# Performance work log

Hardware: AMD Instinct MI355X
Metric: run time of the kernel (lower is better)

Reference implementation:

```python
import jax, jax.numpy as jnp
from jax import lax
import numpy as np

GROUPS = 32

def setup_inputs() -> dict:
    key = jax.random.key(0)
    ks = jax.random.split(key, 12)
    B, C, H, O, N = 4, 256, 256, 256, 4096
    s = 0.02  # small init scale to keep logits in a stable range
    x  = jax.random.normal(ks[0], (B, C, N), dtype=jnp.float32)
    Wk = jax.random.normal(ks[1], (H, C), dtype=jnp.float32) * s
    bk = jax.random.normal(ks[2], (H,), dtype=jnp.float32) * s
    Wq = jax.random.normal(ks[3], (H, C), dtype=jnp.float32) * s
    bq = jax.random.normal(ks[4], (H,), dtype=jnp.float32) * s
    W1 = jax.random.normal(ks[5], (H, C), dtype=jnp.float32) * s
    b1 = jax.random.normal(ks[6], (H,), dtype=jnp.float32) * s
    # grouped conv1d kernel: (out_ch, in_ch // groups, kw) in 'OIH' layout
    W2 = jax.random.normal(ks[7], (H, H // GROUPS, 3), dtype=jnp.float32) * s
    b2 = jax.random.normal(ks[8], (H,), dtype=jnp.float32) * s
    W3 = jax.random.normal(ks[9], (O, H), dtype=jnp.float32) * s
    b3 = jax.random.normal(ks[10], (O,), dtype=jnp.float32) * s
    return {"x": x, "Wk": Wk, "bk": bk, "Wq": Wq, "bq": bq,
            "W1": W1, "b1": b1, "W2": W2, "b2": b2, "W3": W3, "b3": b3}


def reference(x, Wk, bk, Wq, bq, W1, b1, W2, b2, W3, b3):
    # k: 1x1 conv then permute(0,2,1) -> [B, N, H]
    k = jnp.einsum('hc,bcn->bnh', Wk, x) + bk
    # q: 1x1 conv -> [B, H, N]
    q = jnp.einsum('hc,bcn->bhn', Wq, x) + bq[None, :, None]
    # sim = softmax(k @ q, dim=-2): softmax over the FIRST N axis (rows)
    sim = jax.nn.softmax(jnp.einsum('bnh,bhm->bnm', k, q), axis=-2)  # [B, N, N]
    # v path: 1x1 conv -> grouped 3-tap conv (pad=1) -> ReLU -> 1x1 conv
    v1 = jnp.einsum('hc,bcn->bhn', W1, x) + b1[None, :, None]
    v2 = lax.conv_general_dilated(
        v1, W2, window_strides=(1,), padding='SAME',
        feature_group_count=GROUPS,
        dimension_numbers=('NCH', 'OIH', 'NCH')) + b2[None, :, None]
    v2 = jax.nn.relu(v2)
    v = jnp.einsum('oh,bhn->bon', W3, v2) + b3[None, :, None]  # [B, O, N]
    # out = v @ sim -> [B, O, N]
    return jnp.einsum('bon,bnm->bom', v, sim)
```

## Files before the change

kernel.cpp:

```cpp
#include <hip/hip_runtime.h>


#define B_ 4
#define C_ 256
#define H_ 256
#define O_ 256
#define N_ 4096
#define NSPLIT 4
#define SPAN (N_ / NSPLIT)
#define ITERS (SPAN / 32)

typedef short short8 __attribute__((ext_vector_type(8)));
typedef float floatx4 __attribute__((ext_vector_type(4)));
typedef float floatx16 __attribute__((ext_vector_type(16)));
typedef unsigned uint2v __attribute__((ext_vector_type(2)));

__device__ __forceinline__ unsigned short f2bf(float f) {
  unsigned u = __float_as_uint(f);
  u = (u + 0x7fffu + ((u >> 16) & 1u)) >> 16;
  return (unsigned short)u;
}
__device__ __forceinline__ float bf2f(unsigned short u) {
  return __uint_as_float(((unsigned)u) << 16);
}
__device__ __forceinline__ floatx4 mfma16(short8 a, short8 b, floatx4 c) {
  return __builtin_amdgcn_mfma_f32_16x16x32_bf16(a, b, c, 0, 0, 0);
}
__device__ __forceinline__ floatx16 mfma32(short8 a, short8 b, floatx16 c) {
  return __builtin_amdgcn_mfma_f32_32x32x16_bf16(a, b, c, 0, 0, 0);
}
__device__ __forceinline__ unsigned pack2bf(float a, float b) {
  return __builtin_amdgcn_perm(__float_as_uint(b) + 0x8000u,
                               __float_as_uint(a) + 0x8000u, 0x07060302u);
}

__global__ __launch_bounds__(256) void prep_transpose_kernel(
    const float* __restrict__ x, unsigned short* __restrict__ xt,
    const float* __restrict__ Wk, const float* __restrict__ Wq,
    const float* __restrict__ W1, const float* __restrict__ W3,
    unsigned short* __restrict__ wk, unsigned short* __restrict__ wq,
    unsigned short* __restrict__ w1, unsigned short* __restrict__ w3) {
  __shared__ unsigned short tile[64][66];
  const int gid = blockIdx.x;
  const int t = threadIdx.x;
  if (gid >= 1024) {
    const int i = (gid - 1024) * 256 + t;
    wk[i] = f2bf(Wk[i]);
    wq[i] = f2bf(Wq[i]);
    w1[i] = f2bf(W1[i]);
    w3[i] = f2bf(W3[i]);
    return;
  }
  const int b  = gid >> 8;
  const int ct = (gid >> 6) & 3;
  const int nt = gid & 63;
  const int c0 = ct * 64, n0 = nt * 64;
  const float* xb = x + ((size_t)b * C_ + c0) * N_ + n0;
#pragma unroll
  for (int rr = 0; rr < 4; ++rr) {
    const int c = (t >> 4) + rr * 16;
    const floatx4 v = *reinterpret_cast<const floatx4*>(
        xb + (size_t)c * N_ + (t & 15) * 4);
#pragma unroll
    for (int i = 0; i < 4; ++i) tile[c][(t & 15) * 4 + i] = f2bf(v[i]);
  }
  __syncthreads();
  unsigned short* xo = xt + ((size_t)b * N_ + n0) * C_ + c0;
#pragma unroll
  for (int rr = 0; rr < 2; ++rr) {
    const int nr = (t >> 3) + rr * 32;
    short8 pk;
#pragma unroll
    for (int i = 0; i < 8; ++i) pk[i] = (short)tile[(t & 7) * 8 + i][nr];
    *reinterpret_cast<short8*>(xo + (size_t)nr * C_ + (t & 7) * 8) = pk;
  }
}

__global__ __launch_bounds__(256) void gemm1_kernel(
    const unsigned short* __restrict__ xt,
    const unsigned short* __restrict__ wk, const unsigned short* __restrict__ wq,
    const unsigned short* __restrict__ w1,
    const float* __restrict__ bk, const float* __restrict__ bq,
    const float* __restrict__ b1,
    unsigned short* __restrict__ ko, unsigned short* __restrict__ qo,
    unsigned short* __restrict__ v1o) {
  const int lane = threadIdx.x & 63;
  const int wid  = blockIdx.x * 4 + (threadIdx.x >> 6);
  const int b  = wid >> 9;
  const int r  = wid & 511;
  const int hh = r >> 8;
  const int nt = r & 255;
  const int n0 = nt * 16;
  const int m  = lane & 15;
  const int q  = lane >> 4;

  const unsigned short* xrow = xt + ((size_t)(b * N_) + n0 + m) * C_;
  const unsigned short* Ws[3] = {wk, wq, w1};

  floatx4 acc[3][8];
  const floatx4 z = {0.f, 0.f, 0.f, 0.f};
#pragma unroll
  for (int o = 0; o < 3; ++o)
#pragma unroll
    for (int tt = 0; tt < 8; ++tt) acc[o][tt] = z;

  for (int cs = 0; cs < 8; ++cs) {
    const int cb = cs * 32 + q * 8;
    short8 af = *reinterpret_cast<const short8*>(xrow + cb);
#pragma unroll
    for (int o = 0; o < 3; ++o) {
#pragma unroll
      for (int tt = 0; tt < 8; ++tt) {
        const int h0 = (hh * 8 + tt) * 16;
        short8 bf = *reinterpret_cast<const short8*>(Ws[o] + (h0 + m) * C_ + cb);
        acc[o][tt] = mfma16(af, bf, acc[o][tt]);
      }
    }
  }

#pragma unroll
  for (int tt = 0; tt < 8; ++tt) {
    const int ks16 = hh * 8 + tt;
    const float bias = bk[ks16 * 16 + m];
#pragma unroll
    for (int r2 = 0; r2 < 4; ++r2) {
      const int n = n0 + q * 4 + r2;
      ko[((size_t)(b * 128 + (n >> 5))) * 8192 + ks16 * 512 + (m >> 3) * 256 +
         (n & 31) * 8 + (m & 7)] = f2bf(acc[0][tt][r2] + bias);
    }
  }
  const float* biases[2] = {bq, b1};
  unsigned short* outs[2] = {qo, v1o};
#pragma unroll
  for (int o = 0; o < 2; ++o) {
#pragma unroll
    for (int tt = 0; tt < 8; ++tt) {
      const int h0 = (hh * 8 + tt) * 16;
      const float bias = biases[o][h0 + m];
#pragma unroll
      for (int r2 = 0; r2 < 4; ++r2) {
        const int n = n0 + q * 4 + r2;
        outs[o][(b * N_ + n) * H_ + h0 + m] = f2bf(acc[o + 1][tt][r2] + bias);
      }
    }
  }
}

__global__ __launch_bounds__(256) void convgemm2_kernel(
    const unsigned short* __restrict__ v1, const float* __restrict__ W2,
    const float* __restrict__ b2, const unsigned short* __restrict__ w3,
    const float* __restrict__ b3, unsigned short* __restrict__ vo) {
  __shared__ unsigned short v2L[32][264];

  const int h   = threadIdx.x;
  const int blk = blockIdx.x;
  const int b   = blk >> 7;
  const int nc  = blk & 127;
  const int n0  = nc * 32;
  const int g8  = h & ~7;

  {
    float w[24];
#pragma unroll
    for (int i = 0; i < 24; ++i) w[i] = W2[h * 24 + i];
    const float bias = b2[h];
    const unsigned short* vb = v1 + (size_t)b * (N_ * H_) + g8;

    float fp[8], fc[8], fn[8];
    if (n0 == 0) {
#pragma unroll
      for (int i = 0; i < 8; ++i) fp[i] = 0.f;
    } else {
      short8 u = *reinterpret_cast<const short8*>(vb + (size_t)(n0 - 1) * H_);
#pragma unroll
      for (int i = 0; i < 8; ++i) fp[i] = bf2f((unsigned short)u[i]);
    }
    {
      short8 u = *reinterpret_cast<const short8*>(vb + (size_t)n0 * H_);
#pragma unroll
      for (int i = 0; i < 8; ++i) fc[i] = bf2f((unsigned short)u[i]);
    }
#pragma unroll 1
    for (int ns = 0; ns < 32; ++ns) {
      const int n = n0 + ns;
      if (n + 1 < N_) {
        short8 u = *reinterpret_cast<const short8*>(vb + (size_t)(n + 1) * H_);
#pragma unroll
        for (int i = 0; i < 8; ++i) fn[i] = bf2f((unsigned short)u[i]);
      } else {
#pragma unroll
        for (int i = 0; i < 8; ++i) fn[i] = 0.f;
      }
      float a = bias;
#pragma unroll
      for (int i = 0; i < 8; ++i)
        a += w[i * 3] * fp[i] + w[i * 3 + 1] * fc[i] + w[i * 3 + 2] * fn[i];
      v2L[ns][h] = f2bf(fmaxf(a, 0.f));
#pragma unroll
      for (int i = 0; i < 8; ++i) { fp[i] = fc[i]; fc[i] = fn[i]; }
    }
  }
  __syncthreads();

  const int ln = threadIdx.x & 63;
  const int wv = threadIdx.x >> 6;
  const int m  = ln & 31;
  const int hl = ln >> 5;

  floatx16 acc2[2];
#pragma unroll
  for (int ot = 0; ot < 2; ++ot)
#pragma unroll
    for (int r = 0; r < 16; ++r) acc2[ot][r] = 0.f;

#pragma unroll
  for (int ks = 0; ks < 16; ++ks) {
    short8 bfr = *reinterpret_cast<const short8*>(&v2L[m][ks * 16 + hl * 8]);
#pragma unroll
    for (int ot = 0; ot < 2; ++ot) {
      const int o0 = wv * 64 + ot * 32;
      short8 afr = *reinterpret_cast<const short8*>(
          w3 + (o0 + m) * H_ + ks * 16 + hl * 8);
      acc2[ot] = mfma32(afr, bfr, acc2[ot]);
    }
  }

  const int kn = (m >> 4) & 1;
  const int nl = m & 15;
  unsigned short* vkn = vo + ((size_t)(b * 128 + nc) * 2 + kn) * 4096;
#pragma unroll
  for (int ot = 0; ot < 2; ++ot)
#pragma unroll
    for (int r = 0; r < 16; ++r) {
      const int o = wv * 64 + ot * 32 + (r & 3) + 8 * (r >> 2) + 4 * hl;
      vkn[(o >> 5) * 512 + (nl >> 3) * 256 + (o & 31) * 8 + (nl & 7)] =
          f2bf(acc2[ot][r] + b3[o]);
    }
}

__global__ __launch_bounds__(512, 2) void attn_kernel(
    const unsigned short* __restrict__ kbf, const unsigned short* __restrict__ qbf,
    const unsigned short* __restrict__ vbf,
    unsigned short* __restrict__ pacc, float* __restrict__ pml) {
  __shared__ __attribute__((aligned(16))) char smem[7][16384];

  const int tid = threadIdx.x;
  const int ln  = tid & 63;
  const int wv  = tid >> 6;
  const int gid = blockIdx.x;
  const int b   = gid & 3;
  const int s   = (gid >> 2) & 3;
  const int mt256 = gid >> 4;
  const int mt32  = mt256 * 8 + wv;
  const int m0  = mt32 * 32;
  const int m   = ln & 31;
  const int hl  = ln >> 5;
  const bool grpB = (wv >= 4);
  const int lane_base = ln * 16;

  const unsigned short* qrow = qbf + ((size_t)b * N_ + m0 + m) * H_ + hl * 8;
  short8 qf[16];
#pragma unroll
  for (int ks = 0; ks < 16; ++ks)
    qf[ks] = *reinterpret_cast<const short8*>(qrow + ks * 16);

  floatx16 acc[8];
#pragma unroll
  for (int t = 0; t < 8; ++t)
#pragma unroll
    for (int r = 0; r < 16; ++r) acc[t][r] = 0.f;
  float Lp = 0.f;

  const size_t row0 = (size_t)(b * 128 + s * 32);

  auto stage = [&](int nc) {
    const char* kg = (const char*)(kbf + (row0 + nc) * 8192);
    const char* vg = (const char*)(vbf + (row0 + nc) * 8192);
    char* lk = &smem[nc % 3][0];
    char* lv = &smem[3 + (nc & 3)][0];
#pragma unroll
    for (int j = 0; j < 2; ++j) {
      const int ofs = j * 8192 + tid * 16;
      __builtin_amdgcn_global_load_lds(
          (const __attribute__((address_space(1))) void*)(kg + ofs),
          (__attribute__((address_space(3))) void*)(lk + ofs), 16, 0, 0);
      __builtin_amdgcn_global_load_lds(
          (const __attribute__((address_space(1))) void*)(vg + ofs),
          (__attribute__((address_space(3))) void*)(lv + ofs), 16, 0, 0);
    }
  };

  short8 pf0, pf1;

  auto qk = [&](const char* sk) -> floatx16 {
    floatx16 sacc;
#pragma unroll
    for (int r = 0; r < 16; ++r) sacc[r] = 0.f;
    __builtin_amdgcn_s_setprio(1);
#pragma unroll
    for (int ks = 0; ks < 16; ++ks) {
      short8 kf = *reinterpret_cast<const short8*>(sk + lane_base + ks * 1024);
      sacc = mfma32(kf, qf[ks], sacc);
    }
    __builtin_amdgcn_s_setprio(0);
    return sacc;
  };
  auto pv = [&](const char* sv) {
    __builtin_amdgcn_s_setprio(1);
#pragma unroll
    for (int ot = 0; ot < 8; ++ot) {
      short8 vf0 = *reinterpret_cast<const short8*>(sv + lane_base + ot * 1024);
      short8 vf1 = *reinterpret_cast<const short8*>(
          sv + lane_base + 8192 + ot * 1024);
      acc[ot] = mfma32(vf0, pf0, acc[ot]);
      acc[ot] = mfma32(vf1, pf1, acc[ot]);
    }
    __builtin_amdgcn_s_setprio(0);
  };
  auto softmax = [&](floatx16 sacc) {
#if __has_builtin(__builtin_amdgcn_permlane32_swap)
    unsigned d[8];
#pragma unroll
    for (int i = 0; i < 8; ++i) {
      const float a = __expf(sacc[2 * i]);
      const float bb = __expf(sacc[2 * i + 1]);
      Lp += a + bb;
      d[i] = pack2bf(a, bb);
    }
#pragma unroll
    for (int g = 0; g < 2; ++g) {
      uint2v r0 = __builtin_amdgcn_permlane32_swap(d[4 * g + 0], d[4 * g + 2],
                                                   false, false);
      uint2v r1 = __builtin_amdgcn_permlane32_swap(d[4 * g + 1], d[4 * g + 3],
                                                   false, false);
      d[4 * g + 0] = r0.x; d[4 * g + 2] = r0.y;
      d[4 * g + 1] = r1.x; d[4 * g + 3] = r1.y;
    }
    union { unsigned u[4]; short8 s8; } c0, c1;
    c0.u[0] = d[0]; c0.u[1] = d[1]; c0.u[2] = d[2]; c0.u[3] = d[3];
    c1.u[0] = d[4]; c1.u[1] = d[5]; c1.u[2] = d[6]; c1.u[3] = d[7];
    pf0 = c0.s8;
    pf1 = c1.s8;
#else
    float pv_[16];
#pragma unroll
    for (int r = 0; r < 16; ++r) { pv_[r] = __expf(sacc[r]); Lp += pv_[r]; }
    unsigned wpk[8];
#pragma unroll
    for (int r4 = 0; r4 < 4; ++r4) {
      wpk[r4]     = pack2bf(pv_[r4], pv_[r4 + 4]);
      wpk[r4 + 4] = pack2bf(pv_[r4 + 8], pv_[r4 + 12]);
    }
    const int hlsh = hl * 16;
#pragma unroll
    for (int j = 0; j < 8; ++j) {
      const int srcLane = m + ((j >> 2) << 5);
      const int u0 = __shfl((int)wpk[j & 3],       srcLane);
      const int u1 = __shfl((int)wpk[(j & 3) + 4], srcLane);
      pf0[j] = (short)((unsigned)u0 >> hlsh);
      pf1[j] = (short)((unsigned)u1 >> hlsh);
    }
#endif
  };

  stage(0);
  stage(1);

#pragma unroll 1
  for (int nc = 0; nc < ITERS; ++nc) {
    if (nc + 1 < ITERS) {
      asm volatile("s_waitcnt vmcnt(4)\n\ts_barrier" ::: "memory");
    } else {
      asm volatile("s_waitcnt vmcnt(0)\n\ts_barrier" ::: "memory");
    }
    __builtin_amdgcn_sched_barrier(0);
    if (nc + 2 < ITERS) stage(nc + 2);

    const char* sk = &smem[nc % 3][0];

    if (!grpB) {
      floatx16 sacc = qk(sk);
      softmax(sacc);
      pv(&smem[3 + (nc & 3)][0]);
    } else {
      if (nc > 0) pv(&smem[3 + ((nc - 1) & 3)][0]);
      floatx16 sacc = qk(sk);
      softmax(sacc);
    }
  }
  if (grpB) pv(&smem[3 + ((ITERS - 1) & 3)][0]);

  float Lv = Lp + __shfl_xor(Lp, 32);
  const float invL = 1.f / Lv;

  const int pwid = (b * 128 + mt32) * NSPLIT + s;
  unsigned short* pa = pacc + (size_t)pwid * (O_ * 32);
#pragma unroll
  for (int ot = 0; ot < 8; ++ot)
#pragma unroll
    for (int r = 0; r < 16; ++r) {
      const int o = ot * 32 + (r & 3) + 8 * (r >> 2) + 4 * hl;
      pa[o * 32 + m] = f2bf(acc[ot][r] * invL);
    }
  if (hl == 0) pml[pwid * 32 + m] = Lv;
}

__global__ __launch_bounds__(256) void combine_kernel(
    const unsigned short* __restrict__ pacc, const float* __restrict__ pml,
    float* __restrict__ out) {
  const int blk = blockIdx.x;
  const int b   = blk >> 7;
  const int mw  = blk & 127;
  const int o   = threadIdx.x;
  const int base = (b * 128 + mw) * NSPLIT;

  __shared__ float w[NSPLIT][32];
  if (threadIdx.x < 32) {
    const int c = threadIdx.x;
    float L[NSPLIT], sum = 0.f;
#pragma unroll
    for (int sp = 0; sp < NSPLIT; ++sp) {
      L[sp] = pml[(base + sp) * 32 + c];
      sum += L[sp];
    }
    const float inv = 1.f / sum;
#pragma unroll
    for (int sp = 0; sp < NSPLIT; ++sp) w[sp][c] = L[sp] * inv;
  }
  __syncthreads();

  float res[32];
#pragma unroll
  for (int c = 0; c < 32; ++c) res[c] = 0.f;
#pragma unroll
  for (int sp = 0; sp < NSPLIT; ++sp) {
    const unsigned short* pa =
        pacc + (size_t)(base + sp) * (O_ * 32) + o * 32;
#pragma unroll
    for (int c8 = 0; c8 < 4; ++c8) {
      short8 u = *reinterpret_cast<const short8*>(pa + c8 * 8);
#pragma unroll
      for (int i = 0; i < 8; ++i)
        res[c8 * 8 + i] =
            fmaf(w[sp][c8 * 8 + i], bf2f((unsigned short)u[i]), res[c8 * 8 + i]);
    }
  }
  float* ob = out + ((size_t)(b * O_ + o)) * N_ + mw * 32;
#pragma unroll
  for (int c4 = 0; c4 < 8; ++c4) {
    floatx4 v4 = {res[c4 * 4], res[c4 * 4 + 1], res[c4 * 4 + 2], res[c4 * 4 + 3]};
    *reinterpret_cast<floatx4*>(ob + c4 * 4) = v4;
  }
}

extern "C" void kernel_launch(void* const* d_in, const int* in_sizes, int n_in,
                              void* d_out, int out_size, void* d_ws, size_t ws_size,
                              hipStream_t stream) {
  const float* x  = (const float*)d_in[0];
  const float* Wk = (const float*)d_in[1];
  const float* bk = (const float*)d_in[2];
  const float* Wq = (const float*)d_in[3];
  const float* bq = (const float*)d_in[4];
  const float* W1 = (const float*)d_in[5];
  const float* b1 = (const float*)d_in[6];
  const float* W2 = (const float*)d_in[7];
  const float* b2 = (const float*)d_in[8];
  const float* W3 = (const float*)d_in[9];
  const float* b3 = (const float*)d_in[10];
  float* out = (float*)d_out;

  char* ws = (char*)d_ws;
  const size_t SZ = (size_t)B_ * N_ * H_ * sizeof(unsigned short);
  unsigned short* wkbf = (unsigned short*)(ws);
  unsigned short* wqbf = (unsigned short*)(ws + 131072);
  unsigned short* w1bf = (unsigned short*)(ws + 262144);
  unsigned short* w3bf = (unsigned short*)(ws + 393216);
  char* base = ws + 524288;
  unsigned short* kbf  = (unsigned short*)(base);
  unsigned short* qbf  = (unsigned short*)(base + SZ);
  unsigned short* vbf  = (unsigned short*)(base + 2 * SZ);
  unsigned short* xtbf = (unsigned short*)(base + 3 * SZ);
  unsigned short* v1bf = (unsigned short*)(base + 4 * SZ);
  unsigned short* pacc = (unsigned short*)(base + 3 * SZ);
  float*          pml  = (float*)(base + 7 * SZ);

  prep_transpose_kernel<<<1280, 256, 0, stream>>>(
      x, xtbf, Wk, Wq, W1, W3, wkbf, wqbf, w1bf, w3bf);
  gemm1_kernel<<<512, 256, 0, stream>>>(xtbf, wkbf, wqbf, w1bf, bk, bq, b1,
                                        kbf, qbf, v1bf);
  convgemm2_kernel<<<512, 256, 0, stream>>>(v1bf, W2, b2, w3bf, b3, vbf);
  attn_kernel<<<256, 512, 0, stream>>>(kbf, qbf, vbf, pacc, pml);
  combine_kernel<<<512, 256, 0, stream>>>(pacc, pml, out);
}
```

Before: 242.5 us.

## Replace split partial buffers and combine pass with atomic accumulation plus normalize

The attention kernel now atomically adds unnormalized fp32 per-split accumulators directly into the output and atomically sums the softmax denominators into a separate buffer. Both are zeroed by extra blocks in the prep kernel, and a lightweight normalize kernel then divides each output by its column sum. This removes the bf16 partial-buffer writes and the combine kernel's reads. In exchange it adds global atomic traffic, a zeroing pass and a read-modify-write pass over the full output, and the result now depends on atomic ordering.

```diff
diff --git a/kernel.cpp b/kernel.cpp
--- a/kernel.cpp
+++ b/kernel.cpp
@@ -39,10 +39,26 @@
     const float* __restrict__ Wk, const float* __restrict__ Wq,
     const float* __restrict__ W1, const float* __restrict__ W3,
     unsigned short* __restrict__ wk, unsigned short* __restrict__ wq,
-    unsigned short* __restrict__ w1, unsigned short* __restrict__ w3) {
+    unsigned short* __restrict__ w1, unsigned short* __restrict__ w3,
+    float* __restrict__ out, float* __restrict__ Lsum) {
   __shared__ unsigned short tile[64][66];
   const int gid = blockIdx.x;
   const int t = threadIdx.x;
+  if (gid >= 1536) {
+    const floatx4 z4 = {0.f, 0.f, 0.f, 0.f};
+#pragma unroll
+    for (int p = 0; p < 16; ++p)
+      *reinterpret_cast<floatx4*>(Lsum + (p * 256 + t) * 4) = z4;
+    return;
+  }
+  if (gid >= 1280) {
+    float* ob = out + (size_t)(gid - 1280) * 16384;
+    const floatx4 z4 = {0.f, 0.f, 0.f, 0.f};
+#pragma unroll
+    for (int p = 0; p < 16; ++p)
+      *reinterpret_cast<floatx4*>(ob + (p * 256 + t) * 4) = z4;
+    return;
+  }
   if (gid >= 1024) {
     const int i = (gid - 1024) * 256 + t;
     wk[i] = f2bf(Wk[i]);
@@ -241,7 +257,7 @@
 __global__ __launch_bounds__(512, 2) void attn_kernel(
     const unsigned short* __restrict__ kbf, const unsigned short* __restrict__ qbf,
     const unsigned short* __restrict__ vbf,
-    unsigned short* __restrict__ pacc, float* __restrict__ pml) {
+    float* __restrict__ out, float* __restrict__ Lsum) {
   __shared__ __attribute__((aligned(16))) char smem[7][16384];
 
   const int tid = threadIdx.x;
@@ -391,66 +407,33 @@
   if (grpB) pv(&smem[3 + ((ITERS - 1) & 3)][0]);
 
   float Lv = Lp + __shfl_xor(Lp, 32);
-  const float invL = 1.f / Lv;
-
-  const int pwid = (b * 128 + mt32) * NSPLIT + s;
-  unsigned short* pa = pacc + (size_t)pwid * (O_ * 32);
+
+  float* ob = out + ((size_t)b * O_) * N_ + m0 + m;
 #pragma unroll
   for (int ot = 0; ot < 8; ++ot)
 #pragma unroll
     for (int r = 0; r < 16; ++r) {
       const int o = ot * 32 + (r & 3) + 8 * (r >> 2) + 4 * hl;
-      pa[o * 32 + m] = f2bf(acc[ot][r] * invL);
-    }
-  if (hl == 0) pml[pwid * 32 + m] = Lv;
-}
-
-__global__ __launch_bounds__(256) void combine_kernel(
-    const unsigned short* __restrict__ pacc, const float* __restrict__ pml,
-    float* __restrict__ out) {
+      atomicAdd(ob + (size_t)o * N_, acc[ot][r]);
+    }
+  if (hl == 0) atomicAdd(&Lsum[b * N_ + m0 + m], Lv);
+}
+
+__global__ __launch_bounds__(256) void normalize_kernel(
+    float* __restrict__ out, const float* __restrict__ Lsum) {
   const int blk = blockIdx.x;
-  const int b   = blk >> 7;
-  const int mw  = blk & 127;
-  const int o   = threadIdx.x;
-  const int base = (b * 128 + mw) * NSPLIT;
-
-  __shared__ float w[NSPLIT][32];
-  if (threadIdx.x < 32) {
-    const int c = threadIdx.x;
-    float L[NSPLIT], sum = 0.f;
-#pragma unroll
-    for (int sp = 0; sp < NSPLIT; ++sp) {
-      L[sp] = pml[(base + sp) * 32 + c];
-      sum += L[sp];
-    }
-    const float inv = 1.f / sum;
-#pragma unroll
-    for (int sp = 0; sp < NSPLIT; ++sp) w[sp][c] = L[sp] * inv;
-  }
-  __syncthreads();
-
-  float res[32];
-#pragma unroll
-  for (int c = 0; c < 32; ++c) res[c] = 0.f;
-#pragma unroll
-  for (int sp = 0; sp < NSPLIT; ++sp) {
-    const unsigned short* pa =
-        pacc + (size_t)(base + sp) * (O_ * 32) + o * 32;
-#pragma unroll
-    for (int c8 = 0; c8 < 4; ++c8) {
-      short8 u = *reinterpret_cast<const short8*>(pa + c8 * 8);
-#pragma unroll
-      for (int i = 0; i < 8; ++i)
-        res[c8 * 8 + i] =
-            fmaf(w[sp][c8 * 8 + i], bf2f((unsigned short)u[i]), res[c8 * 8 + i]);
-    }
-  }
-  float* ob = out + ((size_t)(b * O_ + o)) * N_ + mw * 32;
-#pragma unroll
-  for (int c4 = 0; c4 < 8; ++c4) {
-    floatx4 v4 = {res[c4 * 4], res[c4 * 4 + 1], res[c4 * 4 + 2], res[c4 * 4 + 3]};
-    *reinterpret_cast<floatx4*>(ob + c4 * 4) = v4;
-  }
+  const int b   = blk >> 10;
+  const int rem = blk & 1023;
+  const int o   = rem >> 2;
+  const int nq  = rem & 3;
+  const int n   = nq * 1024 + threadIdx.x * 4;
+
+  const floatx4 L = *reinterpret_cast<const floatx4*>(&Lsum[b * N_ + n]);
+  float* p = out + ((size_t)(b * O_ + o)) * N_ + n;
+  floatx4 v = *reinterpret_cast<const floatx4*>(p);
+#pragma unroll
+  for (int i = 0; i < 4; ++i) v[i] *= __builtin_amdgcn_rcpf(L[i]);
+  *reinterpret_cast<floatx4*>(p) = v;
 }
 
 extern "C" void kernel_launch(void* const* d_in, const int* in_sizes, int n_in,
@@ -481,14 +464,13 @@
   unsigned short* vbf  = (unsigned short*)(base + 2 * SZ);
   unsigned short* xtbf = (unsigned short*)(base + 3 * SZ);
   unsigned short* v1bf = (unsigned short*)(base + 4 * SZ);
-  unsigned short* pacc = (unsigned short*)(base + 3 * SZ);
-  float*          pml  = (float*)(base + 7 * SZ);
-
-  prep_transpose_kernel<<<1280, 256, 0, stream>>>(
-      x, xtbf, Wk, Wq, W1, W3, wkbf, wqbf, w1bf, w3bf);
+  float*          Lsum = (float*)(base + 7 * SZ);
+
+  prep_transpose_kernel<<<1537, 256, 0, stream>>>(
+      x, xtbf, Wk, Wq, W1, W3, wkbf, wqbf, w1bf, w3bf, out, Lsum);
   gemm1_kernel<<<512, 256, 0, stream>>>(xtbf, wkbf, wqbf, w1bf, bk, bq, b1,
                                         kbf, qbf, v1bf);
   convgemm2_kernel<<<512, 256, 0, stream>>>(v1bf, W2, b2, w3bf, b3, vbf);
-  attn_kernel<<<256, 512, 0, stream>>>(kbf, qbf, vbf, pacc, pml);
-  combine_kernel<<<512, 256, 0, stream>>>(pacc, pml, out);
-}
+  attn_kernel<<<256, 512, 0, stream>>>(kbf, qbf, vbf, out, Lsum);
+  normalize_kernel<<<4096, 256, 0, stream>>>(out, Lsum);
+}
```

After: 274.4 us. 1.13x slower.
